# Optimization experiments

Measured on AMD Instinct MI355X. Metric: run time of the kernel, lower is better.

## Reference

```python
import jax, jax.numpy as jnp
import numpy as np

WS = 7   # window_size
SS = 3   # shift_size = window_size // 2
NH = 16  # num_heads


def _rel_pos_index(ws):
    coords = np.stack(np.meshgrid(np.arange(ws), np.arange(ws), indexing='ij'))  # (2, ws, ws)
    cf = coords.reshape(2, -1)
    rel = (cf[:, :, None] - cf[:, None, :]).transpose(1, 2, 0)
    rel[:, :, 0] += ws - 1
    rel[:, :, 1] += ws - 1
    rel[:, :, 0] *= 2 * ws - 1
    return rel.sum(-1)  # (ws*ws, ws*ws) int

REL_IDX = _rel_pos_index(WS)


def _attn_mask(h, w, ws, ss):
    img = np.zeros((h, w))
    sls = (slice(0, -ws), slice(-ws, -ss), slice(-ss, None))
    cnt = 0
    for i in sls:
        for j in sls:
            img[i, j] = cnt
            cnt += 1
    mw = img.reshape(h // ws, ws, w // ws, ws).transpose(0, 2, 1, 3).reshape(-1, ws * ws)
    d = mw[:, None, :] - mw[:, :, None]  # (nW, N, N)
    return np.where(d != 0, -100.0, 0.0).astype(np.float32)


def _part(x, ws):
    b, h, w, c = x.shape
    return x.reshape(b, h // ws, ws, w // ws, ws, c).transpose(0, 1, 3, 2, 4, 5).reshape(-1, ws * ws, c)


def _rev(win, ws, h, w):
    c = win.shape[-1]
    b = win.shape[0] // ((h // ws) * (w // ws))
    return win.reshape(b, h // ws, w // ws, ws, ws, c).transpose(0, 1, 3, 2, 4, 5).reshape(b, h, w, c)


def _ln(x, g, b):
    m = x.mean(-1, keepdims=True)
    v = x.var(-1, keepdims=True)
    return (x - m) / jnp.sqrt(v + 1e-5) * g + b


def _wattn(x, qkv_w, qkv_b, proj_w, proj_b, table, mask):
    B_, N, C = x.shape
    hd = C // NH
    scale = hd ** -0.5
    qkv = (x @ qkv_w.T + qkv_b).reshape(B_, N, 3, NH, hd).transpose(2, 0, 3, 1, 4)
    q, k, v = qkv[0] * scale, qkv[1], qkv[2]  # (B_, NH, N, hd)
    attn = jnp.einsum('bhnd,bhmd->bhnm', q, k)
    bias = table[REL_IDX.reshape(-1)].reshape(N, N, NH).transpose(2, 0, 1)  # (NH, N, N)
    attn = attn + bias[None]
    if mask is not None:
        nW = mask.shape[0]
        attn = (attn.reshape(B_ // nW, nW, NH, N, N) + mask[None, :, None]).reshape(B_, NH, N, N)
    attn = jax.nn.softmax(attn, axis=-1)
    out = jnp.einsum('bhnm,bhmd->bhnd', attn, v).transpose(0, 2, 1, 3).reshape(B_, N, C)
    return out @ proj_w.T + proj_b


def _mlp(x, w1, b1, w2, b2):
    return jax.nn.gelu(x @ w1.T + b1, approximate=False) @ w2.T + b2


def _forward(x, w_norm1_g, w_norm1_b, w_qkv_w, w_qkv_b, w_proj_w, w_proj_b, w_table,
             w_norm2_g, w_norm2_b, w_fc1_w, w_fc1_b, w_fc2_w, w_fc2_b,
             sw_norm1_g, sw_norm1_b, sw_qkv_w, sw_qkv_b, sw_proj_w, sw_proj_b, sw_table,
             sw_norm2_g, sw_norm2_b, sw_fc1_w, sw_fc1_b, sw_fc2_w, sw_fc2_b):
    b, c, h, w = x.shape
    x = jnp.transpose(x, (0, 2, 3, 1)).reshape(b, h * w, c)  # (B, HW, C)
    shortcut = x
    xn = _ln(x, w_norm1_g, w_norm1_b).reshape(b, h, w, c)
    aw = _wattn(_part(xn, WS), w_qkv_w, w_qkv_b, w_proj_w, w_proj_b, w_table, None)
    x = shortcut + _rev(aw, WS, h, w).reshape(b, h * w, c)
    x = x + _mlp(_ln(x, w_norm2_g, w_norm2_b), w_fc1_w, w_fc1_b, w_fc2_w, w_fc2_b)
    # shifted-window branch (shift_size > 0 since min(h,w) > window_size)
    xn = _ln(x, sw_norm1_g, sw_norm1_b)
    mask = jnp.asarray(_attn_mask(h, w, WS, SS))
    shifted = jnp.roll(xn.reshape(b, h, w, c), (-SS, -SS), axis=(1, 2))
    sa = _wattn(_part(shifted, WS), sw_qkv_w, sw_qkv_b, sw_proj_w, sw_proj_b, sw_table, mask)
    shifted = jnp.roll(_rev(sa, WS, h, w), (SS, SS), axis=(1, 2)).reshape(b, h * w, c)
    # NOTE: source adds the residual to the *normalized* activations here; kept faithful.
    x = xn + shifted
    x = x + _mlp(_ln(x, sw_norm2_g, sw_norm2_b), sw_fc1_w, sw_fc1_b, sw_fc2_w, sw_fc2_b)
    return x.reshape(b, h, w, c)


def setup_inputs() -> dict:
    key = jax.random.key(0)
    ks = jax.random.split(key, 32)
    B, C, H, W = 8, 512, 56, 56
    Cm = 4 * C
    T = (2 * WS - 1) ** 2

    def rn(k, shape, s=0.02):
        return jax.random.normal(k, shape, jnp.float32) * s

    d = {'x': jax.random.normal(ks[0], (B, C, H, W), jnp.float32)}
    for i, p in enumerate(['w', 'sw']):
        o = 1 + i * 6
        d[p + '_norm1_g'] = jnp.ones((C,), jnp.float32)
        d[p + '_norm1_b'] = jnp.zeros((C,), jnp.float32)
        d[p + '_qkv_w'] = rn(ks[o], (3 * C, C))
        d[p + '_qkv_b'] = jnp.zeros((3 * C,), jnp.float32)
        d[p + '_proj_w'] = rn(ks[o + 1], (C, C))
        d[p + '_proj_b'] = jnp.zeros((C,), jnp.float32)
        d[p + '_table'] = rn(ks[o + 2], (T, NH))
        d[p + '_norm2_g'] = jnp.ones((C,), jnp.float32)
        d[p + '_norm2_b'] = jnp.zeros((C,), jnp.float32)
        d[p + '_fc1_w'] = rn(ks[o + 3], (Cm, C))
        d[p + '_fc1_b'] = jnp.zeros((Cm,), jnp.float32)
        d[p + '_fc2_w'] = rn(ks[o + 4], (C, Cm))
        d[p + '_fc2_b'] = jnp.zeros((C,), jnp.float32)
    return d


def reference(x, w_norm1_g, w_norm1_b, w_qkv_w, w_qkv_b, w_proj_w, w_proj_b, w_table,
              w_norm2_g, w_norm2_b, w_fc1_w, w_fc1_b, w_fc2_w, w_fc2_b,
              sw_norm1_g, sw_norm1_b, sw_qkv_w, sw_qkv_b, sw_proj_w, sw_proj_b, sw_table,
              sw_norm2_g, sw_norm2_b, sw_fc1_w, sw_fc1_b, sw_fc2_w, sw_fc2_b):
    return _forward(x, w_norm1_g, w_norm1_b, w_qkv_w, w_qkv_b, w_proj_w, w_proj_b, w_table,
                    w_norm2_g, w_norm2_b, w_fc1_w, w_fc1_b, w_fc2_w, w_fc2_b,
                    sw_norm1_g, sw_norm1_b, sw_qkv_w, sw_qkv_b, sw_proj_w, sw_proj_b, sw_table,
                    sw_norm2_g, sw_norm2_b, sw_fc1_w, sw_fc1_b, sw_fc2_w, sw_fc2_b)
```

## Files before the change

### kernel.cpp

```cpp
#include <hip/hip_runtime.h>
#include <hip/hip_bf16.h>

using bf16 = __hip_bfloat16;

#define B_      8
#define C_      512
#define H_      56
#define W_      56
#define HW_     3136
#define M_      25088
#define NH_     16
#define HD_     32
#define WS_     7
#define NT_     49

typedef __attribute__((ext_vector_type(8))) short bf16x8;
typedef __attribute__((ext_vector_type(4))) float f32x4;

#define AS1(p) ((const __attribute__((address_space(1))) void*)(p))
#define AS3(p) ((__attribute__((address_space(3))) void*)(p))

__device__ inline float bf2f(const bf16 v) {
    unsigned short u = *reinterpret_cast<const unsigned short*>(&v);
    return __uint_as_float((unsigned)u << 16);
}
__device__ inline unsigned short f2bfu(float f) {
    bf16 h = __float2bfloat16(f);
    return *reinterpret_cast<unsigned short*>(&h);
}
__device__ inline float rdv(const float* p) { return *p; }
__device__ inline float rdv(const bf16* p)  { return bf2f(*p); }
__device__ inline void stv(float* p, float v) { *p = v; }
__device__ inline void stv(bf16* p, float v)  { *p = __float2bfloat16(v); }

__global__ void k_detect(const void* g1, int* flag) {
    const unsigned short* u = (const unsigned short*)g1;
    *flag = (u[0] == 0x3F80u) ? 1 : 0;
}

struct WArgs {
    const void* src[26];
    bf16*       dst[26];
    int         n[26];
};
__global__ __launch_bounds__(256) void k_convert_all(WArgs a, const int* flag) {
    const int isb = *flag;
    const int gid = blockIdx.x * 256 + threadIdx.x;
    const int stride = gridDim.x * 256;
    #pragma unroll 1
    for (int w = 0; w < 26; ++w) {
        const int n = a.n[w];
        bf16* d = a.dst[w];
        if (isb) {
            const unsigned short* s = (const unsigned short*)a.src[w];
            for (int i = gid; i < n; i += stride) ((unsigned short*)d)[i] = s[i];
        } else {
            const float* s = (const float*)a.src[w];
            for (int i = gid; i < n; i += stride) d[i] = __float2bfloat16(s[i]);
        }
    }
}

__global__ __launch_bounds__(256) void k_transpose_in(const void* xin, float* X,
                                                      const int* flag) {
    __shared__ float tile[32][33];
    const int isb = *flag;
    const int p0 = blockIdx.x * 32, c0 = blockIdx.y * 32, b = blockIdx.z;
    const int tp = threadIdx.x & 31, tc = threadIdx.x >> 5;
    const size_t ibase = (size_t)b * C_ * HW_;
    #pragma unroll
    for (int i = 0; i < 4; ++i) {
        const int c = tc + i * 8;
        const size_t idx = ibase + (size_t)(c0 + c) * HW_ + p0 + tp;
        tile[c][tp] = isb ? bf2f(((const bf16*)xin)[idx]) : ((const float*)xin)[idx];
    }
    __syncthreads();
    const int wc = threadIdx.x & 31, wp = threadIdx.x >> 5;
    float* dst = X + (size_t)b * HW_ * C_;
    #pragma unroll
    for (int i = 0; i < 4; ++i) {
        const int p = wp + i * 8;
        dst[(size_t)(p0 + p) * C_ + c0 + wc] = tile[wc][p];
    }
}

__global__ __launch_bounds__(128) void k_layernorm(const float* __restrict__ X,
                                                   const bf16* __restrict__ g,
                                                   const bf16* __restrict__ bta,
                                                   bf16* __restrict__ XN) {
    const int tok = blockIdx.x;
    const float4 v = reinterpret_cast<const float4*>(X + (size_t)tok * C_)[threadIdx.x];
    float s  = v.x + v.y + v.z + v.w;
    float s2 = v.x * v.x + v.y * v.y + v.z * v.z + v.w * v.w;
    #pragma unroll
    for (int o = 32; o > 0; o >>= 1) { s += __shfl_down(s, o); s2 += __shfl_down(s2, o); }
    __shared__ float sh[4];
    if ((threadIdx.x & 63) == 0) { sh[threadIdx.x >> 6] = s; sh[2 + (threadIdx.x >> 6)] = s2; }
    __syncthreads();
    const float ts = sh[0] + sh[1], ts2 = sh[2] + sh[3];
    const float m = ts * (1.0f / C_);
    const float var = ts2 * (1.0f / C_) - m * m;
    const float r = rsqrtf(var + 1e-5f);
    const int c = threadIdx.x * 4;
    ushort4 o;
    o.x = f2bfu((v.x - m) * r * bf2f(g[c + 0]) + bf2f(bta[c + 0]));
    o.y = f2bfu((v.y - m) * r * bf2f(g[c + 1]) + bf2f(bta[c + 1]));
    o.z = f2bfu((v.z - m) * r * bf2f(g[c + 2]) + bf2f(bta[c + 2]));
    o.w = f2bfu((v.w - m) * r * bf2f(g[c + 3]) + bf2f(bta[c + 3]));
    reinterpret_cast<ushort4*>(XN + (size_t)tok * C_)[threadIdx.x] = o;
}

template <typename TADD, typename TO, bool GELU, bool ADD, bool FINAL>
__global__ __launch_bounds__(256, 2) void k_gemm_mfma(const bf16* __restrict__ A,
                                                      const bf16* __restrict__ Wt,
                                                      const bf16* __restrict__ bias,
                                                      const TADD* __restrict__ addp,
                                                      TO* __restrict__ out,
                                                      const int* flag,
                                                      int rowBase, int N, int K) {
    __shared__ bf16 sA[2][128 * 64];
    __shared__ bf16 sB[2][128 * 64];
    const int tid  = threadIdx.x;
    const int lane = tid & 63;
    const int wid  = tid >> 6;
    const int wr   = wid >> 1;
    const int wc2  = wid & 1;
    const int m0 = blockIdx.y * 128, n0 = blockIdx.x * 128;

    const f32x4 vz = {0.f, 0.f, 0.f, 0.f};
    f32x4 acc[4][4];
    #pragma unroll
    for (int i = 0; i < 4; ++i)
        #pragma unroll
        for (int j = 0; j < 4; ++j) acc[i][j] = vz;

    const int sr8  = lane >> 3;
    const int schk = (lane & 7) ^ sr8;
    const bf16* gA0 = A  + (size_t)(m0 + sr8) * K + schk * 8;
    const bf16* gB0 = Wt + (size_t)(n0 + sr8) * K + schk * 8;

    const int l15 = lane & 15, g4 = lane >> 4;
    const int NTLE = K >> 6;

    int cur = 0;
    {
        #pragma unroll
        for (int p = 0; p < 4; ++p) {
            const int q = wid * 4 + p;
            __builtin_amdgcn_global_load_lds(AS1(gA0 + (size_t)(q * 8) * K),
                                             AS3(&sA[0][q * 512]), 16, 0, 0);
            __builtin_amdgcn_global_load_lds(AS1(gB0 + (size_t)(q * 8) * K),
                                             AS3(&sB[0][q * 512]), 16, 0, 0);
        }
    }

    for (int t = 0; t < NTLE; ++t) {
        asm volatile("s_waitcnt vmcnt(0)" ::: "memory");
        __builtin_amdgcn_s_barrier();

        if (t + 1 < NTLE) {
            const int kt = (t + 1) << 6;
            #pragma unroll
            for (int p = 0; p < 4; ++p) {
                const int q = wid * 4 + p;
                __builtin_amdgcn_global_load_lds(AS1(gA0 + (size_t)(q * 8) * K + kt),
                                                 AS3(&sA[cur ^ 1][q * 512]), 16, 0, 0);
                __builtin_amdgcn_global_load_lds(AS1(gB0 + (size_t)(q * 8) * K + kt),
                                                 AS3(&sB[cur ^ 1][q * 512]), 16, 0, 0);
            }
        }

        bf16x8 af[4][2], bf_[4][2];
        #pragma unroll
        for (int ks = 0; ks < 2; ++ks) {
            const int ch = ((ks << 2) | g4) ^ (l15 & 7);
            #pragma unroll
            for (int f = 0; f < 4; ++f) {
                const int rowA = wr * 64 + f * 16 + l15;
                af[f][ks] = *reinterpret_cast<const bf16x8*>(&sA[cur][rowA * 64 + ch * 8]);
                const int rowB = wc2 * 64 + f * 16 + l15;
                bf_[f][ks] = *reinterpret_cast<const bf16x8*>(&sB[cur][rowB * 64 + ch * 8]);
            }
        }

        __builtin_amdgcn_s_setprio(1);
        #pragma unroll
        for (int i = 0; i < 4; ++i)
            #pragma unroll
            for (int j = 0; j < 4; ++j) {
                acc[i][j] = __builtin_amdgcn_mfma_f32_16x16x32_bf16(af[i][0], bf_[j][0], acc[i][j], 0, 0, 0);
                acc[i][j] = __builtin_amdgcn_mfma_f32_16x16x32_bf16(af[i][1], bf_[j][1], acc[i][j], 0, 0, 0);
            }
        __builtin_amdgcn_s_setprio(0);

        asm volatile("s_waitcnt lgkmcnt(0)" ::: "memory");
        __builtin_amdgcn_s_barrier();
        cur ^= 1;
    }

    int obf = 0;
    if constexpr (FINAL) obf = *flag;
    const int colBase = n0 + wc2 * 64 + l15;
    const int rowTop  = rowBase + m0 + wr * 64 + g4 * 4;
    #pragma unroll
    for (int j = 0; j < 4; ++j) {
        const int col = colBase + j * 16;
        const float bc = bf2f(bias[col]);
        #pragma unroll
        for (int i = 0; i < 4; ++i) {
            #pragma unroll
            for (int r = 0; r < 4; ++r) {
                const int row = rowTop + i * 16 + r;
                float v = acc[i][j][r] + bc;
                if constexpr (GELU) v = 0.5f * v * (1.0f + erff(v * 0.70710678118654752f));
                if constexpr (ADD)  v += rdv(&addp[(size_t)row * N + col]);
                if constexpr (FINAL) {
                    if (obf) ((bf16*)(void*)out)[(size_t)row * N + col] = __float2bfloat16(v);
                    else     ((float*)(void*)out)[(size_t)row * N + col] = v;
                } else {
                    stv(&out[(size_t)row * N + col], v);
                }
            }
        }
    }
}

__global__ __launch_bounds__(256) void k_mktbl(const bf16* __restrict__ table,
                                               bf16* __restrict__ out, int shifted) {
    const int bh = blockIdx.x;
    const int cls = bh >> 4, h = bh & 15;
    const int rowE = shifted ? (cls >> 1) : 0;
    const int colE = shifted ? (cls & 1) : 0;
    for (int e = threadIdx.x; e < 64 * 64; e += 256) {
        const int i = e >> 6, j = e & 63;
        float v;
        if (i < NT_ && j < NT_) {
            const int yi = i / WS_, xi = i % WS_, yj = j / WS_, xj = j % WS_;
            const int ridx = (yi - yj + 6) * 13 + (xi - xj + 6);
            v = bf2f(table[ridx * NH_ + h]);
            const int ri = (rowE ? (yi < 4 ? 1 : 2) : 0) * 3 + (colE ? (xi < 4 ? 1 : 2) : 0);
            const int rj = (rowE ? (yj < 4 ? 1 : 2) : 0) * 3 + (colE ? (xj < 4 ? 1 : 2) : 0);
            if (ri != rj) v -= 100.f;
        } else if (j >= NT_) {
            v = -3e30f;
        } else {
            v = 0.f;
        }
        out[((size_t)bh << 12) + e] = __float2bfloat16(v);
    }
}

template <int SS, bool SHIFTED>
__global__ __launch_bounds__(64) void k_attn_mfma(const bf16* __restrict__ QKV,
                                                  const bf16* __restrict__ tbl,
                                                  bf16* __restrict__ O) {
    __shared__ __align__(16) short uQK[5120];
    __shared__ __align__(16) short uVt[2304];
    __shared__ int toks[NT_];
    short* Qs = uQK;
    short* Ks = uQK + 2560;
    short* Ps = uQK;

    const int lane = threadIdx.x;
    const int head = blockIdx.x & 15;
    const int win  = blockIdx.x >> 4;
    const int bl = win >> 6, w64 = win & 63;
    const int wy = w64 >> 3, wx = w64 & 7;

    if (lane < NT_) {
        const int dy = lane / WS_, dx = lane % WS_;
        const int sr = wy * WS_ + dy, scn = wx * WS_ + dx;
        const int r = (sr + SS) % H_, c = (scn + SS) % W_;
        toks[lane] = bl * HW_ + r * W_ + c;
    }
    __syncthreads();

    const int g4 = lane >> 4, l15 = lane & 15;
    const int tsg = lane >> 2, csg = (lane & 3) * 8;

    #pragma unroll
    for (int rr = 0; rr < 4; ++rr) {
        const int t = rr * 16 + tsg;
        bf16x8 qv = {0,0,0,0,0,0,0,0}, kv = {0,0,0,0,0,0,0,0}, vv = {0,0,0,0,0,0,0,0};
        if (t < NT_) {
            const bf16* base = QKV + (size_t)toks[t] * 1536 + head * HD_ + csg;
            qv = *reinterpret_cast<const bf16x8*>(base);
            kv = *reinterpret_cast<const bf16x8*>(base + 512);
            vv = *reinterpret_cast<const bf16x8*>(base + 1024);
        }
        *reinterpret_cast<bf16x8*>(&Qs[t * 40 + csg]) = qv;
        *reinterpret_cast<bf16x8*>(&Ks[t * 40 + csg]) = kv;
        #pragma unroll
        for (int e = 0; e < 8; ++e) uVt[(csg + e) * 72 + t] = ((const short*)&vv)[e];
    }
    __syncthreads();

    bf16x8 aq[4], bk[4];
    #pragma unroll
    for (int f = 0; f < 4; ++f) {
        aq[f] = *reinterpret_cast<const bf16x8*>(&Qs[(f * 16 + l15) * 40 + g4 * 8]);
        bk[f] = *reinterpret_cast<const bf16x8*>(&Ks[(f * 16 + l15) * 40 + g4 * 8]);
    }
    const f32x4 vz = {0.f, 0.f, 0.f, 0.f};
    f32x4 sacc[4][4];
    #pragma unroll
    for (int qi = 0; qi < 4; ++qi)
        #pragma unroll
        for (int kj = 0; kj < 4; ++kj)
            sacc[qi][kj] = __builtin_amdgcn_mfma_f32_16x16x32_bf16(aq[qi], bk[kj], vz, 0, 0, 0);
    __syncthreads();

    const int cls = SHIFTED ? (((wy == 7) ? 2 : 0) + ((wx == 7) ? 1 : 0)) : 0;
    const bf16* tb = tbl + (((size_t)(cls * NH_ + head)) << 12);
    const float scale = 0.17677669529663687f;
    #pragma unroll
    for (int qi = 0; qi < 4; ++qi) {
        #pragma unroll
        for (int r = 0; r < 4; ++r) {
            const int i = qi * 16 + g4 * 4 + r;
            const bf16* trow = tb + (i << 6);
            float sv[4];
            #pragma unroll
            for (int kj = 0; kj < 4; ++kj)
                sv[kj] = sacc[qi][kj][r] * scale + bf2f(trow[kj * 16 + l15]);
            float mx = fmaxf(fmaxf(sv[0], sv[1]), fmaxf(sv[2], sv[3]));
            #pragma unroll
            for (int d = 1; d <= 8; d <<= 1) mx = fmaxf(mx, __shfl_xor(mx, d));
            float p[4], sum = 0.f;
            #pragma unroll
            for (int kj = 0; kj < 4; ++kj) { p[kj] = __expf(sv[kj] - mx); sum += p[kj]; }
            #pragma unroll
            for (int d = 1; d <= 8; d <<= 1) sum += __shfl_xor(sum, d);
            const float inv = 1.0f / sum;
            #pragma unroll
            for (int kj = 0; kj < 4; ++kj)
                Ps[i * 72 + kj * 16 + l15] = (short)f2bfu(p[kj] * inv);
        }
    }
    __syncthreads();

    f32x4 oacc[4][2];
    #pragma unroll
    for (int qi = 0; qi < 4; ++qi) { oacc[qi][0] = vz; oacc[qi][1] = vz; }
    #pragma unroll
    for (int ks = 0; ks < 2; ++ks) {
        bf16x8 bv[2];
        #pragma unroll
        for (int dj = 0; dj < 2; ++dj)
            bv[dj] = *reinterpret_cast<const bf16x8*>(&uVt[(dj * 16 + l15) * 72 + ks * 32 + g4 * 8]);
        #pragma unroll
        for (int qi = 0; qi < 4; ++qi) {
            const bf16x8 ap = *reinterpret_cast<const bf16x8*>(&Ps[(qi * 16 + l15) * 72 + ks * 32 + g4 * 8]);
            #pragma unroll
            for (int dj = 0; dj < 2; ++dj)
                oacc[qi][dj] = __builtin_amdgcn_mfma_f32_16x16x32_bf16(ap, bv[dj], oacc[qi][dj], 0, 0, 0);
        }
    }
    #pragma unroll
    for (int qi = 0; qi < 4; ++qi) {
        #pragma unroll
        for (int r = 0; r < 4; ++r) {
            const int i = qi * 16 + g4 * 4 + r;
            if (i < NT_) {
                const size_t ob = (size_t)toks[i] * C_ + head * HD_ + l15;
                O[ob]      = __float2bfloat16(oacc[qi][0][r]);
                O[ob + 16] = __float2bfloat16(oacc[qi][1][r]);
            }
        }
    }
}

extern "C" void kernel_launch(void* const* d_in, const int* in_sizes, int n_in,
                              void* d_out, int out_size, void* d_ws, size_t ws_size,
                              hipStream_t stream) {
    (void)out_size;
    char* ws = (char*)d_ws;
    const size_t WEIGHT_RESERVE = 12651520;
    bf16*  WC   = (bf16*)ws;
    int*   FLG  = (int*)(ws + WEIGHT_RESERVE);
    bf16*  TBL1 = (bf16*)(ws + WEIGHT_RESERVE + 1024);
    bf16*  TBL2 = (bf16*)(ws + WEIGHT_RESERVE + 1024 + 131072);
    float* X    = (float*)(ws + WEIGHT_RESERVE + 656384);
    bf16*  XN   = (bf16*)((char*)X + (size_t)M_ * C_ * 4);
    char*  BIG  = (char*)XN + (size_t)M_ * C_ * 2;

    const size_t full_need = WEIGHT_RESERVE + 656384 + (size_t)M_ * C_ * 6 + (size_t)M_ * 2048 * 2;
    const int IMGS = (ws_size >= full_need) ? B_ : 2;
    const int NCHUNK = B_ / IMGS;
    const int ROWS = IMGS * HW_;

    size_t offs[27];
    size_t off = 0;
    for (int i = 1; i < n_in && i < 27; ++i) { offs[i] = off; off += (size_t)((in_sizes[i] + 7) & ~7); }
    auto wc = [&](int i) { return (const bf16*)(WC + offs[i]); };

    k_detect<<<1, 1, 0, stream>>>(d_in[1], FLG);
    {
        WArgs a;
        for (int i = 1; i < 27; ++i) {
            a.src[i - 1] = d_in[i];
            a.dst[i - 1] = WC + offs[i];
            a.n[i - 1]   = in_sizes[i];
        }
        k_convert_all<<<512, 256, 0, stream>>>(a, FLG);
    }
    k_mktbl<<<16, 256, 0, stream>>>(wc(7),  TBL1, 0);
    k_mktbl<<<64, 256, 0, stream>>>(wc(20), TBL2, 1);

    const dim3 gT(HW_ / 32, C_ / 32, B_);
    k_transpose_in<<<gT, 256, 0, stream>>>(d_in[0], X, FLG);

    bf16* QKV = (bf16*)BIG;
    bf16* ATT = (bf16*)(BIG + (size_t)ROWS * 1536 * 2);
    bf16* HID = (bf16*)BIG;

    const dim3 gQ(1536 / 128, ROWS / 128);
    const dim3 gP(512 / 128,  ROWS / 128);
    const dim3 gF(2048 / 128, ROWS / 128);
    const dim3 gA(IMGS * 64 * NH_);

    k_layernorm<<<M_, 128, 0, stream>>>(X, wc(1), wc(2), XN);
    for (int c = 0; c < NCHUNK; ++c) {
        const size_t ro = (size_t)c * ROWS;
        k_gemm_mfma<float, bf16, false, false, false><<<gQ, 256, 0, stream>>>(
            XN + ro * C_, wc(3), wc(4), (const float*)nullptr, QKV, nullptr, 0, 1536, C_);
        k_attn_mfma<0, false><<<gA, 64, 0, stream>>>(QKV, TBL1, ATT);
        k_gemm_mfma<float, float, false, true, false><<<gP, 256, 0, stream>>>(
            ATT, wc(5), wc(6), X, X, nullptr, (int)ro, C_, C_);
    }
    k_layernorm<<<M_, 128, 0, stream>>>(X, wc(8), wc(9), XN);
    for (int c = 0; c < NCHUNK; ++c) {
        const size_t ro = (size_t)c * ROWS;
        k_gemm_mfma<float, bf16, true, false, false><<<gF, 256, 0, stream>>>(
            XN + ro * C_, wc(10), wc(11), (const float*)nullptr, HID, nullptr, 0, 2048, C_);
        k_gemm_mfma<float, float, false, true, false><<<gP, 256, 0, stream>>>(
            HID, wc(12), wc(13), X, X, nullptr, (int)ro, C_, 2048);
    }
    k_layernorm<<<M_, 128, 0, stream>>>(X, wc(14), wc(15), XN);
    for (int c = 0; c < NCHUNK; ++c) {
        const size_t ro = (size_t)c * ROWS;
        k_gemm_mfma<float, bf16, false, false, false><<<gQ, 256, 0, stream>>>(
            XN + ro * C_, wc(16), wc(17), (const float*)nullptr, QKV, nullptr, 0, 1536, C_);
        k_attn_mfma<3, true><<<gA, 64, 0, stream>>>(QKV, TBL2, ATT);
        k_gemm_mfma<bf16, float, false, true, false><<<gP, 256, 0, stream>>>(
            ATT, wc(18), wc(19), XN, X, nullptr, (int)ro, C_, C_);
    }
    k_layernorm<<<M_, 128, 0, stream>>>(X, wc(21), wc(22), XN);
    for (int c = 0; c < NCHUNK; ++c) {
        const size_t ro = (size_t)c * ROWS;
        k_gemm_mfma<float, bf16, true, false, false><<<gF, 256, 0, stream>>>(
            XN + ro * C_, wc(23), wc(24), (const float*)nullptr, HID, nullptr, 0, 2048, C_);
        k_gemm_mfma<float, float, false, true, true><<<gP, 256, 0, stream>>>(
            HID, wc(25), wc(26), X, (float*)d_out, FLG, (int)ro, C_, 2048);
    }
}
```

Measured before the change: 852.6 us.

## Store residual stream in bf16 and remap GEMM blocks across XCDs

The residual activation buffer X changes from fp32 to bf16, which halves the traffic in the transpose, layernorm and residual-add GEMM epilogues. GEMM grids also become 1D with an XCD-aware remapping of block indices, so neighbouring tiles land on the same chiplet and share L2 reuse. The bf16 residual loses precision across the four residual additions, which could push results past the accuracy tolerance.

```diff
diff --git a/kernel.cpp b/kernel.cpp
--- a/kernel.cpp
+++ b/kernel.cpp
@@ -61,7 +61,7 @@
     }
 }
 
-__global__ __launch_bounds__(256) void k_transpose_in(const void* xin, float* X,
+__global__ __launch_bounds__(256) void k_transpose_in(const void* xin, bf16* X,
                                                       const int* flag) {
     __shared__ float tile[32][33];
     const int isb = *flag;
@@ -76,20 +76,25 @@
     }
     __syncthreads();
     const int wc = threadIdx.x & 31, wp = threadIdx.x >> 5;
-    float* dst = X + (size_t)b * HW_ * C_;
+    bf16* dst = X + (size_t)b * HW_ * C_;
     #pragma unroll
     for (int i = 0; i < 4; ++i) {
         const int p = wp + i * 8;
-        dst[(size_t)(p0 + p) * C_ + c0 + wc] = tile[wc][p];
-    }
-}
-
-__global__ __launch_bounds__(128) void k_layernorm(const float* __restrict__ X,
+        dst[(size_t)(p0 + p) * C_ + c0 + wc] = __float2bfloat16(tile[wc][p]);
+    }
+}
+
+__global__ __launch_bounds__(128) void k_layernorm(const bf16* __restrict__ X,
                                                    const bf16* __restrict__ g,
                                                    const bf16* __restrict__ bta,
                                                    bf16* __restrict__ XN) {
     const int tok = blockIdx.x;
-    const float4 v = reinterpret_cast<const float4*>(X + (size_t)tok * C_)[threadIdx.x];
+    const ushort4 u = reinterpret_cast<const ushort4*>(X + (size_t)tok * C_)[threadIdx.x];
+    float4 v;
+    v.x = __uint_as_float((unsigned)u.x << 16);
+    v.y = __uint_as_float((unsigned)u.y << 16);
+    v.z = __uint_as_float((unsigned)u.z << 16);
+    v.w = __uint_as_float((unsigned)u.w << 16);
     float s  = v.x + v.y + v.z + v.w;
     float s2 = v.x * v.x + v.y * v.y + v.z * v.z + v.w * v.w;
     #pragma unroll
@@ -125,7 +130,14 @@
     const int wid  = tid >> 6;
     const int wr   = wid >> 1;
     const int wc2  = wid & 1;
-    const int m0 = blockIdx.y * 128, n0 = blockIdx.x * 128;
+
+    const int nwg  = gridDim.x;
+    const int orig = blockIdx.x;
+    const int nx = nwg >> 3, rr_ = nwg & 7;
+    const int xcd = orig & 7, offw = orig >> 3;
+    const int wg = (xcd < rr_ ? xcd * (nx + 1) : rr_ * (nx + 1) + (xcd - rr_) * nx) + offw;
+    const int gx = N >> 7;
+    const int m0 = (wg / gx) * 128, n0 = (wg % gx) * 128;
 
     const f32x4 vz = {0.f, 0.f, 0.f, 0.f};
     f32x4 acc[4][4];
@@ -380,11 +392,11 @@
     int*   FLG  = (int*)(ws + WEIGHT_RESERVE);
     bf16*  TBL1 = (bf16*)(ws + WEIGHT_RESERVE + 1024);
     bf16*  TBL2 = (bf16*)(ws + WEIGHT_RESERVE + 1024 + 131072);
-    float* X    = (float*)(ws + WEIGHT_RESERVE + 656384);
-    bf16*  XN   = (bf16*)((char*)X + (size_t)M_ * C_ * 4);
-    char*  BIG  = (char*)XN + (size_t)M_ * C_ * 2;
-
-    const size_t full_need = WEIGHT_RESERVE + 656384 + (size_t)M_ * C_ * 6 + (size_t)M_ * 2048 * 2;
+    bf16*  X    = (bf16*)(ws + WEIGHT_RESERVE + 656384);
+    bf16*  XN   = X + (size_t)M_ * C_;
+    char*  BIG  = (char*)(XN + (size_t)M_ * C_);
+
+    const size_t full_need = WEIGHT_RESERVE + 656384 + (size_t)M_ * C_ * 4 + (size_t)M_ * 2048 * 2;
     const int IMGS = (ws_size >= full_need) ? B_ : 2;
     const int NCHUNK = B_ / IMGS;
     const int ROWS = IMGS * HW_;
@@ -414,43 +426,43 @@
     bf16* ATT = (bf16*)(BIG + (size_t)ROWS * 1536 * 2);
     bf16* HID = (bf16*)BIG;
 
-    const dim3 gQ(1536 / 128, ROWS / 128);
-    const dim3 gP(512 / 128,  ROWS / 128);
-    const dim3 gF(2048 / 128, ROWS / 128);
+    const int gQ = (1536 / 128) * (ROWS / 128);
+    const int gP = (512 / 128)  * (ROWS / 128);
+    const int gF = (2048 / 128) * (ROWS / 128);
     const dim3 gA(IMGS * 64 * NH_);
 
     k_layernorm<<<M_, 128, 0, stream>>>(X, wc(1), wc(2), XN);
     for (int c = 0; c < NCHUNK; ++c) {
         const size_t ro = (size_t)c * ROWS;
-        k_gemm_mfma<float, bf16, false, false, false><<<gQ, 256, 0, stream>>>(
-            XN + ro * C_, wc(3), wc(4), (const float*)nullptr, QKV, nullptr, 0, 1536, C_);
+        k_gemm_mfma<bf16, bf16, false, false, false><<<gQ, 256, 0, stream>>>(
+            XN + ro * C_, wc(3), wc(4), (const bf16*)nullptr, QKV, nullptr, 0, 1536, C_);
         k_attn_mfma<0, false><<<gA, 64, 0, stream>>>(QKV, TBL1, ATT);
-        k_gemm_mfma<float, float, false, true, false><<<gP, 256, 0, stream>>>(
+        k_gemm_mfma<bf16, bf16, false, true, false><<<gP, 256, 0, stream>>>(
             ATT, wc(5), wc(6), X, X, nullptr, (int)ro, C_, C_);
     }
     k_layernorm<<<M_, 128, 0, stream>>>(X, wc(8), wc(9), XN);
     for (int c = 0; c < NCHUNK; ++c) {
         const size_t ro = (size_t)c * ROWS;
-        k_gemm_mfma<float, bf16, true, false, false><<<gF, 256, 0, stream>>>(
-            XN + ro * C_, wc(10), wc(11), (const float*)nullptr, HID, nullptr, 0, 2048, C_);
-        k_gemm_mfma<float, float, false, true, false><<<gP, 256, 0, stream>>>(
+        k_gemm_mfma<bf16, bf16, true, false, false><<<gF, 256, 0, stream>>>(
+            XN + ro * C_, wc(10), wc(11), (const bf16*)nullptr, HID, nullptr, 0, 2048, C_);
+        k_gemm_mfma<bf16, bf16, false, true, false><<<gP, 256, 0, stream>>>(
             HID, wc(12), wc(13), X, X, nullptr, (int)ro, C_, 2048);
     }
     k_layernorm<<<M_, 128, 0, stream>>>(X, wc(14), wc(15), XN);
     for (int c = 0; c < NCHUNK; ++c) {
         const size_t ro = (size_t)c * ROWS;
-        k_gemm_mfma<float, bf16, false, false, false><<<gQ, 256, 0, stream>>>(
-            XN + ro * C_, wc(16), wc(17), (const float*)nullptr, QKV, nullptr, 0, 1536, C_);
+        k_gemm_mfma<bf16, bf16, false, false, false><<<gQ, 256, 0, stream>>>(
+            XN + ro * C_, wc(16), wc(17), (const bf16*)nullptr, QKV, nullptr, 0, 1536, C_);
         k_attn_mfma<3, true><<<gA, 64, 0, stream>>>(QKV, TBL2, ATT);
-        k_gemm_mfma<bf16, float, false, true, false><<<gP, 256, 0, stream>>>(
+        k_gemm_mfma<bf16, bf16, false, true, false><<<gP, 256, 0, stream>>>(
             ATT, wc(18), wc(19), XN, X, nullptr, (int)ro, C_, C_);
     }
     k_layernorm<<<M_, 128, 0, stream>>>(X, wc(21), wc(22), XN);
     for (int c = 0; c < NCHUNK; ++c) {
         const size_t ro = (size_t)c * ROWS;
-        k_gemm_mfma<float, bf16, true, false, false><<<gF, 256, 0, stream>>>(
-            XN + ro * C_, wc(23), wc(24), (const float*)nullptr, HID, nullptr, 0, 2048, C_);
-        k_gemm_mfma<float, float, false, true, true><<<gP, 256, 0, stream>>>(
+        k_gemm_mfma<bf16, bf16, true, false, false><<<gF, 256, 0, stream>>>(
+            XN + ro * C_, wc(23), wc(24), (const bf16*)nullptr, HID, nullptr, 0, 2048, C_);
+        k_gemm_mfma<bf16, float, false, true, true><<<gP, 256, 0, stream>>>(
             HID, wc(25), wc(26), X, (float*)d_out, FLG, (int)ro, C_, 2048);
     }
 }
```

After: 796.5 us. 1.07x faster.
